# Kernel optimization log

Measured on AMD Instinct MI355X. Metric: run time of the kernel, lower is better.

## Reference

```python
import jax, jax.numpy as jnp
import numpy as np

F = 200      # number of independent feature MLPs
D_IN = 3
H = 15       # enc_out // 2
ENC = 30     # enc_out
B = 32768


def setup_inputs() -> dict:
    key = jax.random.key(0)
    ky, k1, kb1, k2, kb2, k3, kb3 = jax.random.split(key, 7)
    y = jax.random.normal(ky, (B, F, D_IN), dtype=jnp.float32)
    # Per-feature MLP params, stacked along feature axis (grouped GEMM form).
    W1 = jax.random.normal(k1, (F, D_IN, H), dtype=jnp.float32) * (1.0 / np.sqrt(D_IN))
    b1 = jax.random.normal(kb1, (F, H), dtype=jnp.float32) * 0.01
    W2 = jax.random.normal(k2, (F, H, ENC), dtype=jnp.float32) * (1.0 / np.sqrt(H))
    b2 = jax.random.normal(kb2, (F, ENC), dtype=jnp.float32) * 0.01
    # Final linear over the concatenated [F*ENC] vector.
    W3 = jax.random.normal(k3, (F * ENC, 1), dtype=jnp.float32) * (1.0 / np.sqrt(F * ENC))
    b3 = jax.random.normal(kb3, (1,), dtype=jnp.float32) * 0.01
    return {"y": y, "W1": W1, "b1": b1, "W2": W2, "b2": b2, "W3": W3, "b3": b3}


def reference(y, W1, b1, W2, b2, W3, b3):
    # 200 independent tiny MLPs -> one batched einsum per layer.
    h = jax.nn.relu(jnp.einsum('bfi,fih->bfh', y, W1) + b1)      # [B, F, H]
    h = jax.nn.relu(jnp.einsum('bfh,fhe->bfe', h, W2) + b2)      # [B, F, ENC]
    # torch.cat(res, 1) with res[i] = block_i(y[:, i, :]) == reshape [B, F*ENC]
    flat = h.reshape(h.shape[0], F * ENC)
    return flat @ W3 + b3                                         # [B, 1]
```

## Files before the change

### kernel.cpp

```cpp
#include <hip/hip_runtime.h>
#include <hip/hip_bf16.h>

#define NF  200
#define DIN 3
#define NH  15
#define NE  30
#define NB  32768

typedef __attribute__((ext_vector_type(8)))  short short8;
typedef __attribute__((ext_vector_type(16))) float f32x16;

constexpr int FSPLIT = 25;
constexpr int FPW    = NF / FSPLIT;
constexpr int PAIRS  = FPW / 2;
constexpr int BT     = 256;
constexpr int RPW    = 32;
constexpr int RPB    = 4 * RPW;

constexpr size_t OFF_A1P = 0;
constexpr size_t OFF_W2Q = 102400;
constexpr size_t OFF_W3F = 307200;

__device__ __forceinline__ unsigned f2bfu(float x) {
    __hip_bfloat16 h = __float2bfloat16(x);
    unsigned short u; __builtin_memcpy(&u, &h, 2); return (unsigned)u;
}

__device__ __forceinline__ unsigned cvtpk(float lo, float hi) {
    unsigned r;
    asm("v_cvt_pk_bf16_f32 %0, %1, %2" : "=v"(r) : "v"(lo), "v"(hi));
    return r;
}

__device__ __forceinline__ float2 pkfma(float2 a, float2 b, float2 c) {
    float2 d;
    asm("v_pk_fma_f32 %0, %1, %2, %3" : "=v"(d) : "v"(a), "v"(b), "v"(c));
    return d;
}

__global__ void nn_init(float* __restrict__ out, const float* __restrict__ b3) {
    int i = blockIdx.x * 256 + threadIdx.x;
    if (i < NB) out[i] = b3[0];
}

__global__ void nn_prep(const float* __restrict__ W1, const float* __restrict__ b1,
                        const float* __restrict__ W2, const float* __restrict__ b2,
                        const float* __restrict__ W3, char* __restrict__ ws) {
    const int f = blockIdx.x;
    const int t = threadIdx.x;
    const int x = t & 31, hi = t >> 5;
    unsigned short* A1p = (unsigned short*)(ws + OFF_A1P);
    unsigned short* W2q = (unsigned short*)(ws + OFF_W2Q);
    float*          w3f = (float*)(ws + OFF_W3F);

    {
        unsigned short* d = W2q + ((size_t)f * 64 + t) * 8;
#pragma unroll
        for (int j = 0; j < 8; ++j) {
            const int h = (j & 3) + 8 * (j >> 2) + 4 * hi;
            float v = 0.f;
            if (x < NE) v = (h < NH) ? W2[((size_t)f * NH + h) * NE + x]
                                     : b2[f * NE + x];
            d[j] = (unsigned short)f2bfu(v);
        }
    }
    if (t < 32) {
        const int hh = t >> 4, r = t & 15;
        const int e = (r & 3) + 8 * (r >> 2) + 4 * hh;
        w3f[(size_t)f * 32 + t] = (e < NE) ? W3[f * NE + e] : 0.f;
    }

    if ((f & 1) == 0) {
        unsigned short* a = A1p + ((size_t)(f >> 1) * 64 + t) * 8;
#pragma unroll
        for (int j = 0; j < 8; ++j) {
            float v = 0.f;
            if (hi == 0) {
                if (x < 16) {
                    if (x < NH) {
                        if (j < 3)       v = W1[((size_t)f * DIN + j) * NH + x];
                        else if (j == 3) v = b1[f * NH + x];
                    }
                } else {
                    const int h = x - 16;
                    if (h < NH) {
                        if (j >= 4 && j < 7) v = W1[((size_t)(f + 1) * DIN + (j - 4)) * NH + h];
                        else if (j == 7)     v = b1[(f + 1) * NH + h];
                    }
                }
            }
            a[j] = (unsigned short)f2bfu(v);
        }
    }
}

__global__ __launch_bounds__(BT, 3)
void nn_main(const float* __restrict__ y, const char* __restrict__ ws,
             float* __restrict__ out) {
    __shared__ __align__(16) short sA1[PAIRS * 512];
    __shared__ __align__(16) short sW2[FPW * 512];
    __shared__ __align__(16) float sW3f[FPW * 32];

    const int t  = threadIdx.x;
    const int w  = t >> 6;
    const int l  = t & 63;
    const int ln = l & 31;
    const int hi = l >> 5;
    const int r0 = blockIdx.x * RPB + w * RPW;
    const int f0 = blockIdx.y * FPW;
    const int p0 = f0 >> 1;

    const float4* __restrict__ yp4 = reinterpret_cast<const float4*>(
        y + (size_t)(r0 + ln) * (NF * DIN) + (size_t)f0 * DIN);
    const float4 c0 = yp4[0], c1 = yp4[1], c2 = yp4[2];
    const float4 c3 = yp4[3], c4 = yp4[4], c5 = yp4[5];

    {
        const uint4* gA = (const uint4*)(ws + OFF_A1P + (size_t)p0 * 1024);
        const uint4* gW = (const uint4*)(ws + OFF_W2Q + (size_t)f0 * 1024);
        const uint4* g3 = (const uint4*)(ws + OFF_W3F + (size_t)f0 * 128);
        uint4* dA = (uint4*)sA1;
        uint4* dW = (uint4*)sW2;
        uint4* d3 = (uint4*)sW3f;
        dA[t] = gA[t];
        dW[t]       = gW[t];
        dW[t + 256] = gW[t + 256];
        if (t < 64) d3[t] = g3[t];
    }
    __syncthreads();

    const short* __restrict__ a1l = sA1 + l * 8;
    const short* __restrict__ w2l = sW2 + l * 8;

    const unsigned himask = hi ? 0x3F800000u : 0u;
    const float onef = 1.0f;
    const f32x16 zc = {};

    float2 acc0 = {0.f, 0.f};
    float2 acc1 = {0.f, 0.f};

    auto epilogue = [&](const f32x16& d2, const float* __restrict__ wf) {
        float r[16];
#pragma unroll
        for (int i = 0; i < 16; ++i) r[i] = fmaxf(d2[i], 0.f);
        const float4 w0  = ((const float4*)wf)[0];
        const float4 w1  = ((const float4*)wf)[1];
        const float4 w2_ = ((const float4*)wf)[2];
        const float4 w3_ = ((const float4*)wf)[3];
        acc0 = pkfma(float2{r[0],  r[1]},  float2{w0.x,  w0.y},  acc0);
        acc1 = pkfma(float2{r[2],  r[3]},  float2{w0.z,  w0.w},  acc1);
        acc0 = pkfma(float2{r[4],  r[5]},  float2{w1.x,  w1.y},  acc0);
        acc1 = pkfma(float2{r[6],  r[7]},  float2{w1.z,  w1.w},  acc1);
        acc0 = pkfma(float2{r[8],  r[9]},  float2{w2_.x, w2_.y}, acc0);
        acc1 = pkfma(float2{r[10], r[11]}, float2{w2_.z, w2_.w}, acc1);
        acc0 = pkfma(float2{r[12], r[13]}, float2{w3_.x, w3_.y}, acc0);
        acc1 = pkfma(float2{r[14], r[15]}, float2{w3_.z, w3_.w}, acc1);
    };

    auto pair_body = [&](int pp, float y0A, float y1A, float y2A,
                                 float y0B, float y1B, float y2B) {
        const short8 A1  = *reinterpret_cast<const short8*>(a1l + (size_t)pp * 512);
        const short8 W2A = *reinterpret_cast<const short8*>(w2l + (size_t)(2 * pp) * 512);
        const short8 W2B = *reinterpret_cast<const short8*>(w2l + (size_t)(2 * pp + 1) * 512);

        union { unsigned u[4]; short8 s; } B1;
        B1.u[0] = cvtpk(y0A, y1A);
        B1.u[1] = cvtpk(y2A, onef);
        B1.u[2] = cvtpk(y0B, y1B);
        B1.u[3] = cvtpk(y2B, onef);

        const f32x16 d1 = __builtin_amdgcn_mfma_f32_32x32x16_bf16(A1, B1.s, zc, 0, 0, 0);

        union { unsigned u[4]; short8 s; } PA, PB;
#pragma unroll
        for (int i = 0; i < 4; ++i) {
            PA.u[i] = cvtpk(fmaxf(d1[2 * i], 0.f),     fmaxf(d1[2 * i + 1], 0.f));
            PB.u[i] = cvtpk(fmaxf(d1[8 + 2 * i], 0.f), fmaxf(d1[8 + 2 * i + 1], 0.f));
        }
        PA.u[3] |= himask;
        PB.u[3] |= himask;

        const f32x16 dA2 = __builtin_amdgcn_mfma_f32_32x32x16_bf16(W2A, PA.s, zc, 0, 0, 0);
        epilogue(dA2, sW3f + (2 * pp) * 32 + hi * 16);
        const f32x16 dB2 = __builtin_amdgcn_mfma_f32_32x32x16_bf16(W2B, PB.s, zc, 0, 0, 0);
        epilogue(dB2, sW3f + (2 * pp + 1) * 32 + hi * 16);
    };

    pair_body(0, c0.x, c0.y, c0.z,  c0.w, c1.x, c1.y);
    pair_body(1, c1.z, c1.w, c2.x,  c2.y, c2.z, c2.w);
    pair_body(2, c3.x, c3.y, c3.z,  c3.w, c4.x, c4.y);
    pair_body(3, c4.z, c4.w, c5.x,  c5.y, c5.z, c5.w);

    float partial = (acc0.x + acc1.x) + (acc0.y + acc1.y);
    partial += __shfl_xor(partial, 32);
    if (hi == 0) atomicAdd(&out[r0 + ln], partial);
}

extern "C" void kernel_launch(void* const* d_in, const int* in_sizes, int n_in,
                              void* d_out, int out_size, void* d_ws, size_t ws_size,
                              hipStream_t stream) {
    const float* y  = (const float*)d_in[0];
    const float* W1 = (const float*)d_in[1];
    const float* b1 = (const float*)d_in[2];
    const float* W2 = (const float*)d_in[3];
    const float* b2 = (const float*)d_in[4];
    const float* W3 = (const float*)d_in[5];
    const float* b3 = (const float*)d_in[6];
    float* out = (float*)d_out;

    nn_prep<<<dim3(NF), dim3(64), 0, stream>>>(W1, b1, W2, b2, W3, (char*)d_ws);
    nn_init<<<dim3((NB + 255) / 256), dim3(256), 0, stream>>>(out, b3);
    nn_main<<<dim3(NB / RPB, FSPLIT), dim3(BT), 0, stream>>>(
        y, (const char*)d_ws, out);
}
```

Measured before the change: 42.21 us.

## Fuse weight prep into main kernel and replace atomics with partial-sum reduce

Drops the separate prep and init kernels: each main block now converts its own slice of W1/b1/W2/b2/W3 to bf16 fragments directly in shared memory. Per-split partial sums go to a workspace buffer instead of atomicAdd, and a small reduce kernel adds the splits plus bias. This cuts launches and atomic contention. In exchange, weight conversion is repeated in every block and the partials add an extra round trip through global memory.

```diff
diff --git a/kernel.cpp b/kernel.cpp
--- a/kernel.cpp
+++ b/kernel.cpp
@@ -17,10 +17,6 @@
 constexpr int RPW    = 32;
 constexpr int RPB    = 4 * RPW;
 
-constexpr size_t OFF_A1P = 0;
-constexpr size_t OFF_W2Q = 102400;
-constexpr size_t OFF_W3F = 307200;
-
 __device__ __forceinline__ unsigned f2bfu(float x) {
     __hip_bfloat16 h = __float2bfloat16(x);
     unsigned short u; __builtin_memcpy(&u, &h, 2); return (unsigned)u;
@@ -38,68 +34,14 @@
     return d;
 }
 
-__global__ void nn_init(float* __restrict__ out, const float* __restrict__ b3) {
-    int i = blockIdx.x * 256 + threadIdx.x;
-    if (i < NB) out[i] = b3[0];
-}
-
-__global__ void nn_prep(const float* __restrict__ W1, const float* __restrict__ b1,
-                        const float* __restrict__ W2, const float* __restrict__ b2,
-                        const float* __restrict__ W3, char* __restrict__ ws) {
-    const int f = blockIdx.x;
-    const int t = threadIdx.x;
-    const int x = t & 31, hi = t >> 5;
-    unsigned short* A1p = (unsigned short*)(ws + OFF_A1P);
-    unsigned short* W2q = (unsigned short*)(ws + OFF_W2Q);
-    float*          w3f = (float*)(ws + OFF_W3F);
-
-    {
-        unsigned short* d = W2q + ((size_t)f * 64 + t) * 8;
-#pragma unroll
-        for (int j = 0; j < 8; ++j) {
-            const int h = (j & 3) + 8 * (j >> 2) + 4 * hi;
-            float v = 0.f;
-            if (x < NE) v = (h < NH) ? W2[((size_t)f * NH + h) * NE + x]
-                                     : b2[f * NE + x];
-            d[j] = (unsigned short)f2bfu(v);
-        }
-    }
-    if (t < 32) {
-        const int hh = t >> 4, r = t & 15;
-        const int e = (r & 3) + 8 * (r >> 2) + 4 * hh;
-        w3f[(size_t)f * 32 + t] = (e < NE) ? W3[f * NE + e] : 0.f;
-    }
-
-    if ((f & 1) == 0) {
-        unsigned short* a = A1p + ((size_t)(f >> 1) * 64 + t) * 8;
-#pragma unroll
-        for (int j = 0; j < 8; ++j) {
-            float v = 0.f;
-            if (hi == 0) {
-                if (x < 16) {
-                    if (x < NH) {
-                        if (j < 3)       v = W1[((size_t)f * DIN + j) * NH + x];
-                        else if (j == 3) v = b1[f * NH + x];
-                    }
-                } else {
-                    const int h = x - 16;
-                    if (h < NH) {
-                        if (j >= 4 && j < 7) v = W1[((size_t)(f + 1) * DIN + (j - 4)) * NH + h];
-                        else if (j == 7)     v = b1[(f + 1) * NH + h];
-                    }
-                }
-            }
-            a[j] = (unsigned short)f2bfu(v);
-        }
-    }
-}
-
 __global__ __launch_bounds__(BT, 3)
-void nn_main(const float* __restrict__ y, const char* __restrict__ ws,
-             float* __restrict__ out) {
-    __shared__ __align__(16) short sA1[PAIRS * 512];
-    __shared__ __align__(16) short sW2[FPW * 512];
-    __shared__ __align__(16) float sW3f[FPW * 32];
+void nn_main(const float* __restrict__ y,  const float* __restrict__ W1,
+             const float* __restrict__ b1, const float* __restrict__ W2,
+             const float* __restrict__ b2, const float* __restrict__ W3,
+             float* __restrict__ P) {
+    __shared__ __align__(16) unsigned short sA1[PAIRS * 512];
+    __shared__ __align__(16) unsigned short sW2[FPW * 512];
+    __shared__ __align__(16) float          sW3f[FPW * 32];
 
     const int t  = threadIdx.x;
     const int w  = t >> 6;
@@ -108,7 +50,6 @@
     const int hi = l >> 5;
     const int r0 = blockIdx.x * RPB + w * RPW;
     const int f0 = blockIdx.y * FPW;
-    const int p0 = f0 >> 1;
 
     const float4* __restrict__ yp4 = reinterpret_cast<const float4*>(
         y + (size_t)(r0 + ln) * (NF * DIN) + (size_t)f0 * DIN);
@@ -116,21 +57,60 @@
     const float4 c3 = yp4[3], c4 = yp4[4], c5 = yp4[5];
 
     {
-        const uint4* gA = (const uint4*)(ws + OFF_A1P + (size_t)p0 * 1024);
-        const uint4* gW = (const uint4*)(ws + OFF_W2Q + (size_t)f0 * 1024);
-        const uint4* g3 = (const uint4*)(ws + OFF_W3F + (size_t)f0 * 128);
-        uint4* dA = (uint4*)sA1;
-        uint4* dW = (uint4*)sW2;
-        uint4* d3 = (uint4*)sW3f;
-        dA[t] = gA[t];
-        dW[t]       = gW[t];
-        dW[t + 256] = gW[t + 256];
-        if (t < 64) d3[t] = g3[t];
+        const int g   = t >> 6;
+        const int lt  = t & 63;
+        const int gx  = lt & 31;
+        const int ghi = lt >> 5;
+
+#pragma unroll
+        for (int rep = 0; rep < 2; ++rep) {
+            const int fl = g + rep * 4;
+            const int f  = f0 + fl;
+            unsigned short* d = sW2 + fl * 512 + lt * 8;
+#pragma unroll
+            for (int j = 0; j < 8; ++j) {
+                const int h = (j & 3) + 8 * (j >> 2) + 4 * ghi;
+                float v = 0.f;
+                if (gx < NE) v = (h < NH) ? W2[((size_t)f * NH + h) * NE + gx]
+                                          : b2[f * NE + gx];
+                d[j] = (unsigned short)f2bfu(v);
+            }
+        }
+        {
+            const int fA = f0 + 2 * g;
+            unsigned short* a = sA1 + g * 512 + lt * 8;
+#pragma unroll
+            for (int j = 0; j < 8; ++j) {
+                float v = 0.f;
+                if (ghi == 0) {
+                    if (gx < 16) {
+                        if (gx < NH) {
+                            if (j < 3)       v = W1[((size_t)fA * DIN + j) * NH + gx];
+                            else if (j == 3) v = b1[fA * NH + gx];
+                        }
+                    } else {
+                        const int h = gx - 16;
+                        if (h < NH) {
+                            if (j >= 4 && j < 7) v = W1[((size_t)(fA + 1) * DIN + (j - 4)) * NH + h];
+                            else if (j == 7)     v = b1[(fA + 1) * NH + h];
+                        }
+                    }
+                }
+                a[j] = (unsigned short)f2bfu(v);
+            }
+        }
+        {
+            const int fl = t >> 5, f = f0 + fl;
+            const int x32 = t & 31;
+            const int hh = x32 >> 4, r = t & 15;
+            const int e = (r & 3) + 8 * (r >> 2) + 4 * hh;
+            sW3f[fl * 32 + x32] = (e < NE) ? W3[f * NE + e] : 0.f;
+        }
     }
     __syncthreads();
 
-    const short* __restrict__ a1l = sA1 + l * 8;
-    const short* __restrict__ w2l = sW2 + l * 8;
+    const unsigned short* __restrict__ a1l = sA1 + l * 8;
+    const unsigned short* __restrict__ w2l = sW2 + l * 8;
 
     const unsigned himask = hi ? 0x3F800000u : 0u;
     const float onef = 1.0f;
@@ -193,7 +173,19 @@
 
     float partial = (acc0.x + acc1.x) + (acc0.y + acc1.y);
     partial += __shfl_xor(partial, 32);
-    if (hi == 0) atomicAdd(&out[r0 + ln], partial);
+    if (hi == 0) {
+        P[(size_t)blockIdx.y * NB + r0 + ln] = partial;
+    }
+}
+
+__global__ __launch_bounds__(256)
+void nn_reduce(const float* __restrict__ P, const float* __restrict__ b3,
+               float* __restrict__ out) {
+    const int i = blockIdx.x * 256 + threadIdx.x;
+    float s = b3[0];
+#pragma unroll
+    for (int k = 0; k < FSPLIT; ++k) s += P[(size_t)k * NB + i];
+    out[i] = s;
 }
 
 extern "C" void kernel_launch(void* const* d_in, const int* in_sizes, int n_in,
@@ -207,9 +199,9 @@
     const float* W3 = (const float*)d_in[5];
     const float* b3 = (const float*)d_in[6];
     float* out = (float*)d_out;
-
-    nn_prep<<<dim3(NF), dim3(64), 0, stream>>>(W1, b1, W2, b2, W3, (char*)d_ws);
-    nn_init<<<dim3((NB + 255) / 256), dim3(256), 0, stream>>>(out, b3);
+    float* P   = (float*)d_ws;
+
     nn_main<<<dim3(NB / RPB, FSPLIT), dim3(BT), 0, stream>>>(
-        y, (const char*)d_ws, out);
-}
+        y, W1, b1, W2, b2, W3, P);
+    nn_reduce<<<dim3(NB / 256), dim3(256), 0, stream>>>(P, b3, out);
+}
```

New measurement: 55.49 us. +31.5%, slower.
